# Kernel tuning notes

Measured on AMD Instinct MI355X. Metric: run time of the kernel, lower is better.

The kernel has to match this reference:

```python
import jax, jax.numpy as jnp
import numpy as np

B, CIN, HIN, WIN = 8192, 16, 6, 6
FM = 64                      # feature_maps
DK = FM // 2                 # 32
DV = FM // 2                 # 32
NH = FM // 2                 # 32 heads -> dkh = dvh = 1
OUT_CH = 5
HID = 128


def _conv2d(x, w, b, stride=1):
    # x: NCHW, w: OIHW, VALID padding (padding=(k-1)//2 = 0 for k=2)
    y = jax.lax.conv_general_dilated(
        x, w, window_strides=(stride, stride), padding='VALID',
        dimension_numbers=('NCHW', 'OIHW', 'NCHW'))
    return y + b[None, :, None, None]


def setup_inputs() -> dict:
    key = jax.random.key(0)
    ks = jax.random.split(key, 13)
    s = 0.1  # small init scale keeps softmax logits well-conditioned
    return {
        'x':      jax.random.normal(ks[0], (B, CIN, HIN, WIN), jnp.float32),
        # AugmentedConv: conv_out (out_channels - dv), qkv conv (2dk+dv), attn 1x1
        'conv_w': jax.random.normal(ks[1], (FM - DV, CIN, 2, 2), jnp.float32) * s,
        'conv_b': jax.random.normal(ks[2], (FM - DV,), jnp.float32) * s,
        'qkv_w':  jax.random.normal(ks[3], (2 * DK + DV, CIN, 2, 2), jnp.float32) * s,
        'qkv_b':  jax.random.normal(ks[4], (2 * DK + DV,), jnp.float32) * s,
        'attn_w': jax.random.normal(ks[5], (DV, DV, 1, 1), jnp.float32) * s,
        'attn_b': jax.random.normal(ks[6], (DV,), jnp.float32) * s,
        # DoubleDense: fm*5*5 -> hid -> hid//2 -> out
        'w1': jax.random.normal(ks[7], (HID, FM * 5 * 5), jnp.float32) * s,
        'b1': jax.random.normal(ks[8], (HID,), jnp.float32) * s,
        'w2': jax.random.normal(ks[9], (HID // 2, HID), jnp.float32) * s,
        'b2': jax.random.normal(ks[10], (HID // 2,), jnp.float32) * s,
        'w3': jax.random.normal(ks[11], (OUT_CH, HID // 2), jnp.float32) * s,
        'b3': jax.random.normal(ks[12], (OUT_CH,), jnp.float32) * s,
    }


def _forward(x, conv_w, conv_b, qkv_w, qkv_b, attn_w, attn_b, w1, b1, w2, b2, w3, b3):
    # ---- AugmentedConv ----
    conv_out = _conv2d(x, conv_w, conv_b)            # [B, FM-DV, 5, 5]
    qkv = _conv2d(x, qkv_w, qkv_b)                   # [B, 2DK+DV, 5, 5]
    b, _, h, w = qkv.shape
    q, k, v = jnp.split(qkv, [DK, 2 * DK], axis=1)
    dkh = DK // NH
    q = q * (dkh ** -0.5)
    flat_q = q.reshape(b, NH, dkh, h * w)            # [B, Nh, dkh, HW]
    flat_k = k.reshape(b, NH, dkh, h * w)
    flat_v = v.reshape(b, NH, DV // NH, h * w)
    # logits = q^T k over head-dim: [B, Nh, HW, HW]
    logits = jnp.einsum('bndi,bndj->bnij', flat_q, flat_k)
    weights = jax.nn.softmax(logits, axis=-1)
    # attn = weights @ v^T -> [B, Nh, HW, dvh]
    attn = jnp.einsum('bnij,bnjd->bnid', weights, flat_v.transpose(0, 1, 3, 2))
    # faithful to torch: raw reshape (B, Nh, dvh, H, W) then combine heads
    attn = attn.reshape(b, NH, DV // NH, h, w).reshape(b, DV, h, w)
    attn = _conv2d(attn, attn_w, attn_b)             # 1x1 conv
    y = jnp.concatenate([conv_out, attn], axis=1)    # [B, FM, 5, 5]
    # ---- ReLU + DoubleDense ----
    y = jax.nn.relu(y).reshape(b, -1)                # [B, FM*25]
    y = jax.nn.relu(y @ w1.T + b1)
    y = jax.nn.relu(y @ w2.T + b2)
    return y @ w3.T + b3                             # [B, OUT_CH]


def reference(x, conv_w, conv_b, qkv_w, qkv_b, attn_w, attn_b, w1, b1, w2, b2, w3, b3):
    return _forward(x, conv_w, conv_b, qkv_w, qkv_b, attn_w, attn_b,
                    w1, b1, w2, b2, w3, b3)
```

## Files before the change

kernel.cpp:

```cpp
#include <hip/hip_runtime.h>
#include <hip/hip_bf16.h>
#include <cstdint>
#include <cstddef>


typedef __attribute__((ext_vector_type(4))) float f32x4;
typedef __attribute__((ext_vector_type(8))) __bf16 bf16x8;
typedef __attribute__((ext_vector_type(4))) __bf16 bf16x4;

#define LOG2E 1.4426950408889634f

__device__ __forceinline__ float fast_exp2(float x) {
#if __has_builtin(__builtin_amdgcn_exp2f)
  return __builtin_amdgcn_exp2f(x);
#else
  return __expf(x * 0.6931471805599453f);
#endif
}

__device__ __forceinline__ f32x4 mfma16(bf16x8 a, bf16x8 b, f32x4 c) {
  return __builtin_amdgcn_mfma_f32_16x16x32_bf16(a, b, c, 0, 0, 0);
}

__global__ __launch_bounds__(256) void prep(
    const float* __restrict__ conv_w, const float* __restrict__ qkv_w,
    const float* __restrict__ w1, const float* __restrict__ w2,
    __hip_bfloat16* __restrict__ wqb, __hip_bfloat16* __restrict__ w1bp,
    __hip_bfloat16* __restrict__ w2b) {
  int i = blockIdx.x * 256 + threadIdx.x;
  if (i < 128 * 1600) {
    int n = i / 1600, r = i - n * 1600;
    int c = r & 63, p = r >> 6;
    w1bp[i] = __float2bfloat16(w1[n * 1600 + c * 25 + p]);
  }
  if (i < 8192) {
    wqb[i] = __float2bfloat16(i < 2048 ? conv_w[i] : qkv_w[i - 2048]);
    w2b[i] = __float2bfloat16(w2[i]);
  }
}

__global__ __launch_bounds__(256) void k1(
    const float* __restrict__ x,
    const float* __restrict__ conv_b, const float* __restrict__ qkv_b,
    const __hip_bfloat16* __restrict__ wqb,
    const float* __restrict__ attn_w, const float* __restrict__ attn_b,
    __hip_bfloat16* __restrict__ act) {
  const int t = threadIdx.x;
  const int lane = t & 63, wave = t >> 6;
  const int l15 = lane & 15, quad = lane >> 4;
  const int b0 = blockIdx.x * 4;

  __shared__ __align__(16) char lds_raw[6400 + 27648];
  __bf16* xs  = (__bf16*)lds_raw;
  __bf16* as_ = (__bf16*)lds_raw;
  __bf16* qs  = (__bf16*)(lds_raw + 6400);

  const float* xb = x + (size_t)b0 * 576;
#pragma unroll
  for (int i = 0; i < 9; ++i) {
    int f = t + i * 256;
    xs[f] = __float2bfloat16(xb[f]);
  }

  bf16x8 bfr[8][2];
#pragma unroll
  for (int nt = 0; nt < 8; ++nt)
#pragma unroll
    for (int ks = 0; ks < 2; ++ks)
      bfr[nt][ks] = *(const bf16x8*)((const __bf16*)wqb + (nt * 16 + l15) * 64 + ks * 32 + quad * 8);
  float bias[8];
#pragma unroll
  for (int nt = 0; nt < 8; ++nt) {
    int ch = nt * 16 + l15;
    bias[nt] = (ch < 32) ? conv_b[ch] : qkv_b[ch - 32];
  }
  __syncthreads();

  for (int mt = wave; mt < 7; mt += 4) {
    int row = mt * 16 + l15;
    int rc = row < 99 ? row : 99;
    int bl = rc / 25, pos = rc - bl * 25;
    int ii = pos / 5, jj = pos - ii * 5;
    const __bf16* xp = xs + bl * 576 + ii * 6 + jj;
    bf16x8 af[2];
#pragma unroll
    for (int ks = 0; ks < 2; ++ks) {
      const __bf16* p0 = xp + (ks * 8 + quad * 2) * 36;
      bf16x8 a;
      a[0] = p0[0];  a[1] = p0[1];  a[2] = p0[6];  a[3] = p0[7];
      a[4] = p0[36]; a[5] = p0[37]; a[6] = p0[42]; a[7] = p0[43];
      af[ks] = a;
    }
    f32x4 acc[8];
#pragma unroll
    for (int nt = 0; nt < 8; ++nt) acc[nt] = (f32x4){0.f, 0.f, 0.f, 0.f};
#pragma unroll
    for (int ks = 0; ks < 2; ++ks)
#pragma unroll
      for (int nt = 0; nt < 8; ++nt)
        acc[nt] = mfma16(af[ks], bfr[nt][ks], acc[nt]);

#pragma unroll
    for (int r = 0; r < 4; ++r) {
      int orow = mt * 16 + quad * 4 + r;
      if (orow < 100) {
        int ob = orow / 25, op = orow - ob * 25;
#pragma unroll
        for (int nt = 0; nt < 8; ++nt) {
          float v = acc[nt][r] + bias[nt];
          if (nt < 2) {
            act[((size_t)(b0 + ob) * 25 + op) * 64 + nt * 16 + l15] =
                __float2bfloat16(fmaxf(v, 0.f));
          } else {
            if (nt == 4 || nt == 5) v *= LOG2E;
            qs[(ob * 96 + (nt - 2) * 16 + l15) * 36 + op] = __float2bfloat16(v);
          }
        }
      }
    }
  }
  __syncthreads();

  {
    const int pair = t & 127, half = t >> 7;
    const int bl = pair >> 5, n = pair & 31;
    const __bf16* qp = qs + (bl * 96 + n) * 36;
    const __bf16* kp = qp + 32 * 36;
    const __bf16* vp = qp + 64 * 36;
    float kl[25], vv[25];
#pragma unroll
    for (int c4 = 0; c4 < 6; ++c4) {
      bf16x4 b = *(const bf16x4*)(kp + c4 * 4);
      bf16x4 c = *(const bf16x4*)(vp + c4 * 4);
#pragma unroll
      for (int z = 0; z < 4; ++z) {
        kl[c4 * 4 + z] = (float)b[z];
        vv[c4 * 4 + z] = (float)c[z];
      }
    }
    kl[24] = (float)kp[24]; vv[24] = (float)vp[24];

    const int i0 = half * 12;
    float qv[13];
    {
      const __bf16* qbase = qp + i0;
      bf16x4 q0 = *(const bf16x4*)(qbase);
      bf16x4 q1 = *(const bf16x4*)(qbase + 4);
      bf16x4 q2 = *(const bf16x4*)(qbase + 8);
#pragma unroll
      for (int z = 0; z < 4; ++z) {
        qv[z] = (float)q0[z]; qv[4 + z] = (float)q1[z]; qv[8 + z] = (float)q2[z];
      }
      qv[12] = (float)qbase[12];
    }

#pragma unroll
    for (int z = 0; z < 13; ++z) {
      const float qi = qv[z];
      float s0 = 0.f, s1 = 0.f, s2 = 0.f, s3 = 0.f, s4 = 0.f;
      float o0 = 0.f, o1 = 0.f, o2 = 0.f, o3 = 0.f, o4 = 0.f;
#pragma unroll
      for (int g = 0; g < 5; ++g) {
        float e0 = fast_exp2(qi * kl[g * 5 + 0]);
        float e1 = fast_exp2(qi * kl[g * 5 + 1]);
        float e2 = fast_exp2(qi * kl[g * 5 + 2]);
        float e3 = fast_exp2(qi * kl[g * 5 + 3]);
        float e4 = fast_exp2(qi * kl[g * 5 + 4]);
        s0 += e0; o0 = __builtin_fmaf(e0, vv[g * 5 + 0], o0);
        s1 += e1; o1 = __builtin_fmaf(e1, vv[g * 5 + 1], o1);
        s2 += e2; o2 = __builtin_fmaf(e2, vv[g * 5 + 2], o2);
        s3 += e3; o3 = __builtin_fmaf(e3, vv[g * 5 + 3], o3);
        s4 += e4; o4 = __builtin_fmaf(e4, vv[g * 5 + 4], o4);
      }
      float ss = ((s0 + s1) + (s2 + s3)) + s4;
      float oo = ((o0 + o1) + (o2 + o3)) + o4;
      as_[(bl * 25 + i0 + z) * 32 + n] = __float2bfloat16(oo * __builtin_amdgcn_rcpf(ss));
    }
  }
  __syncthreads();

  {
    bf16x8 bw[2]; float ab[2];
#pragma unroll
    for (int nt2 = 0; nt2 < 2; ++nt2) {
      int n = nt2 * 16 + l15;
#pragma unroll
      for (int j = 0; j < 8; ++j)
        bw[nt2][j] = (__bf16)__float2bfloat16(attn_w[n * 32 + quad * 8 + j]);
      ab[nt2] = attn_b[n];
    }
    for (int mt = wave; mt < 7; mt += 4) {
      int row = mt * 16 + l15;
      int rc = row < 99 ? row : 99;
      bf16x8 af = *(const bf16x8*)(as_ + rc * 32 + quad * 8);
      f32x4 acc[2];
#pragma unroll
      for (int nt2 = 0; nt2 < 2; ++nt2)
        acc[nt2] = mfma16(af, bw[nt2], (f32x4){0.f, 0.f, 0.f, 0.f});
#pragma unroll
      for (int r = 0; r < 4; ++r) {
        int orow = mt * 16 + quad * 4 + r;
        if (orow < 100) {
          int ob = orow / 25, op = orow - ob * 25;
#pragma unroll
          for (int nt2 = 0; nt2 < 2; ++nt2)
            act[((size_t)(b0 + ob) * 25 + op) * 64 + 32 + nt2 * 16 + l15] =
                __float2bfloat16(fmaxf(acc[nt2][r] + ab[nt2], 0.f));
        }
      }
    }
  }
}

__global__ __launch_bounds__(512) void k2(
    const __hip_bfloat16* __restrict__ act,
    const __hip_bfloat16* __restrict__ w1bp, const float* __restrict__ b1,
    const __hip_bfloat16* __restrict__ w2b, const float* __restrict__ b2,
    const float* __restrict__ w3, const float* __restrict__ b3,
    float* __restrict__ out) {
  const int t = threadIdx.x;
  const int lane = t & 63;
  const int wave = t >> 6;
  const int wm = wave >> 2;
  const int wn = wave & 3;
  const int l15 = lane & 15;
  const int quad = lane >> 4;
  const int b0 = blockIdx.x * 32;

  __shared__ __hip_bfloat16 C1s[32 * 136];
  __shared__ __hip_bfloat16 C2s[32 * 72];

  f32x4 acc0 = {0.f, 0.f, 0.f, 0.f};
  f32x4 acc1 = {0.f, 0.f, 0.f, 0.f};
  const __bf16* aptr  = (const __bf16*)act + (size_t)(b0 + wm * 16 + l15) * 1600 + quad * 8;
  const __bf16* bptr0 = (const __bf16*)w1bp + (size_t)(wn * 32 + l15) * 1600 + quad * 8;
  const __bf16* bptr1 = bptr0 + 16 * 1600;
#pragma unroll 5
  for (int k0 = 0; k0 < 1600; k0 += 32) {
    bf16x8 av  = *(const bf16x8*)(aptr + k0);
    bf16x8 bv0 = *(const bf16x8*)(bptr0 + k0);
    bf16x8 bv1 = *(const bf16x8*)(bptr1 + k0);
    acc0 = mfma16(av, bv0, acc0);
    acc1 = mfma16(av, bv1, acc1);
  }
  {
    const int col0 = wn * 32 + l15;
    const float bias0 = b1[col0];
    const float bias1 = b1[col0 + 16];
#pragma unroll
    for (int r = 0; r < 4; ++r) {
      const int row = wm * 16 + quad * 4 + r;
      C1s[row * 136 + col0]      = __float2bfloat16(fmaxf(acc0[r] + bias0, 0.f));
      C1s[row * 136 + col0 + 16] = __float2bfloat16(fmaxf(acc1[r] + bias1, 0.f));
    }
  }
  __syncthreads();

  f32x4 acc2 = {0.f, 0.f, 0.f, 0.f};
  {
    const __bf16* aL = (const __bf16*)C1s + (wm * 16 + l15) * 136 + quad * 8;
    const __bf16* bL = (const __bf16*)w2b + (wn * 16 + l15) * 128 + quad * 8;
#pragma unroll
    for (int k0 = 0; k0 < 128; k0 += 32)
      acc2 = mfma16(*(const bf16x8*)(aL + k0), *(const bf16x8*)(bL + k0), acc2);
  }
  {
    const int col = wn * 16 + l15;
    const float bias = b2[col];
#pragma unroll
    for (int r = 0; r < 4; ++r) {
      const int row = wm * 16 + quad * 4 + r;
      C2s[row * 72 + col] = __float2bfloat16(fmaxf(acc2[r] + bias, 0.f));
    }
  }
  __syncthreads();

  if (t < 160) {
    const int row = t / 5;
    const int oc = t - row * 5;
    float s = b3[oc];
#pragma unroll
    for (int k = 0; k < 64; ++k)
      s += __bfloat162float(C2s[row * 72 + k]) * w3[oc * 64 + k];
    out[(size_t)(b0 + row) * 5 + oc] = s;
  }
}

extern "C" void kernel_launch(void* const* d_in, const int* in_sizes, int n_in,
                              void* d_out, int out_size, void* d_ws, size_t ws_size,
                              hipStream_t stream) {
  const float* x      = (const float*)d_in[0];
  const float* conv_w = (const float*)d_in[1];
  const float* conv_b = (const float*)d_in[2];
  const float* qkv_w  = (const float*)d_in[3];
  const float* qkv_b  = (const float*)d_in[4];
  const float* attn_w = (const float*)d_in[5];
  const float* attn_b = (const float*)d_in[6];
  const float* w1 = (const float*)d_in[7];
  const float* b1 = (const float*)d_in[8];
  const float* w2 = (const float*)d_in[9];
  const float* b2 = (const float*)d_in[10];
  const float* w3 = (const float*)d_in[11];
  const float* b3 = (const float*)d_in[12];
  float* out = (float*)d_out;

  char* ws = (char*)d_ws;
  __hip_bfloat16* act  = (__hip_bfloat16*)ws;
  __hip_bfloat16* w1bp = (__hip_bfloat16*)(ws + 26214400);
  __hip_bfloat16* w2b  = (__hip_bfloat16*)(ws + 26624000);
  __hip_bfloat16* wqb  = (__hip_bfloat16*)(ws + 26640384);

  prep<<<dim3(800), dim3(256), 0, stream>>>(conv_w, qkv_w, w1, w2, wqb, w1bp, w2b);
  k1<<<dim3(2048), dim3(256), 0, stream>>>(x, conv_b, qkv_b, wqb, attn_w, attn_b, act);
  k2<<<dim3(256), dim3(512), 0, stream>>>(act, w1bp, b1, w2b, b2, w3, b3, out);
}
```

Before: 177.3 us.

## Fold weight prep kernel into k1 and shrink attention LDS stride

Removes the separate prep launch. The first 160 blocks of k1 now convert w1 (with its permutation) and w2 to bf16. Every block converts its conv/qkv weight fragments directly from fp32 global memory instead of reading a pre-converted buffer. The q/k/v LDS row stride drops from 36 to 28 elements, which shrinks shared memory and may raise occupancy, and the softmax loop now runs exactly 12 or 13 rows per half instead of always 13. The cost is extra fp32 loads and conversions per block, and some load imbalance on the blocks that also convert weights.

```diff
diff --git a/kernel.cpp b/kernel.cpp
--- a/kernel.cpp
+++ b/kernel.cpp
@@ -22,39 +22,37 @@
   return __builtin_amdgcn_mfma_f32_16x16x32_bf16(a, b, c, 0, 0, 0);
 }
 
-__global__ __launch_bounds__(256) void prep(
-    const float* __restrict__ conv_w, const float* __restrict__ qkv_w,
-    const float* __restrict__ w1, const float* __restrict__ w2,
-    __hip_bfloat16* __restrict__ wqb, __hip_bfloat16* __restrict__ w1bp,
-    __hip_bfloat16* __restrict__ w2b) {
-  int i = blockIdx.x * 256 + threadIdx.x;
-  if (i < 128 * 1600) {
-    int n = i / 1600, r = i - n * 1600;
-    int c = r & 63, p = r >> 6;
-    w1bp[i] = __float2bfloat16(w1[n * 1600 + c * 25 + p]);
-  }
-  if (i < 8192) {
-    wqb[i] = __float2bfloat16(i < 2048 ? conv_w[i] : qkv_w[i - 2048]);
-    w2b[i] = __float2bfloat16(w2[i]);
-  }
-}
-
 __global__ __launch_bounds__(256) void k1(
     const float* __restrict__ x,
-    const float* __restrict__ conv_b, const float* __restrict__ qkv_b,
-    const __hip_bfloat16* __restrict__ wqb,
+    const float* __restrict__ conv_w, const float* __restrict__ conv_b,
+    const float* __restrict__ qkv_w,  const float* __restrict__ qkv_b,
     const float* __restrict__ attn_w, const float* __restrict__ attn_b,
-    __hip_bfloat16* __restrict__ act) {
+    const float* __restrict__ w1, const float* __restrict__ w2,
+    __hip_bfloat16* __restrict__ act,
+    __hip_bfloat16* __restrict__ w1bp, __hip_bfloat16* __restrict__ w2b) {
   const int t = threadIdx.x;
   const int lane = t & 63, wave = t >> 6;
   const int l15 = lane & 15, quad = lane >> 4;
   const int b0 = blockIdx.x * 4;
 
-  __shared__ __align__(16) char lds_raw[6400 + 27648];
+  __shared__ __align__(16) char lds_raw[6400 + 21504];
   __bf16* xs  = (__bf16*)lds_raw;
   __bf16* as_ = (__bf16*)lds_raw;
   __bf16* qs  = (__bf16*)(lds_raw + 6400);
 
+  if (blockIdx.x < 128) {
+    const int n = blockIdx.x;
+    const float* wr = w1 + n * 1600;
+    __hip_bfloat16* wo = w1bp + n * 1600;
+    for (int o = t; o < 1600; o += 256) {
+      int c = o & 63, p = o >> 6;
+      wo[o] = __float2bfloat16(wr[c * 25 + p]);
+    }
+  } else if (blockIdx.x < 160) {
+    int i = (blockIdx.x - 128) * 256 + t;
+    w2b[i] = __float2bfloat16(w2[i]);
+  }
+
   const float* xb = x + (size_t)b0 * 576;
 #pragma unroll
   for (int i = 0; i < 9; ++i) {
@@ -63,16 +61,23 @@
   }
 
   bf16x8 bfr[8][2];
-#pragma unroll
-  for (int nt = 0; nt < 8; ++nt)
-#pragma unroll
-    for (int ks = 0; ks < 2; ++ks)
-      bfr[nt][ks] = *(const bf16x8*)((const __bf16*)wqb + (nt * 16 + l15) * 64 + ks * 32 + quad * 8);
   float bias[8];
 #pragma unroll
   for (int nt = 0; nt < 8; ++nt) {
     int ch = nt * 16 + l15;
+    const float* wrow = (ch < 32) ? (conv_w + ch * 64) : (qkv_w + (ch - 32) * 64);
     bias[nt] = (ch < 32) ? conv_b[ch] : qkv_b[ch - 32];
+#pragma unroll
+    for (int ks = 0; ks < 2; ++ks) {
+      float4 a = *(const float4*)(wrow + ks * 32 + quad * 8);
+      float4 b = *(const float4*)(wrow + ks * 32 + quad * 8 + 4);
+      bf16x8 f;
+      f[0] = (__bf16)__float2bfloat16(a.x); f[1] = (__bf16)__float2bfloat16(a.y);
+      f[2] = (__bf16)__float2bfloat16(a.z); f[3] = (__bf16)__float2bfloat16(a.w);
+      f[4] = (__bf16)__float2bfloat16(b.x); f[5] = (__bf16)__float2bfloat16(b.y);
+      f[6] = (__bf16)__float2bfloat16(b.z); f[7] = (__bf16)__float2bfloat16(b.w);
+      bfr[nt][ks] = f;
+    }
   }
   __syncthreads();
 
@@ -113,7 +118,7 @@
                 __float2bfloat16(fmaxf(v, 0.f));
           } else {
             if (nt == 4 || nt == 5) v *= LOG2E;
-            qs[(ob * 96 + (nt - 2) * 16 + l15) * 36 + op] = __float2bfloat16(v);
+            qs[(ob * 96 + (nt - 2) * 16 + l15) * 28 + op] = __float2bfloat16(v);
           }
         }
       }
@@ -124,9 +129,9 @@
   {
     const int pair = t & 127, half = t >> 7;
     const int bl = pair >> 5, n = pair & 31;
-    const __bf16* qp = qs + (bl * 96 + n) * 36;
-    const __bf16* kp = qp + 32 * 36;
-    const __bf16* vp = qp + 64 * 36;
+    const __bf16* qp = qs + (bl * 96 + n) * 28;
+    const __bf16* kp = qp + 32 * 28;
+    const __bf16* vp = qp + 64 * 28;
     float kl[25], vv[25];
 #pragma unroll
     for (int c4 = 0; c4 < 6; ++c4) {
@@ -154,8 +159,7 @@
       qv[12] = (float)qbase[12];
     }
 
-#pragma unroll
-    for (int z = 0; z < 13; ++z) {
+    auto do_i = [&](int z) {
       const float qi = qv[z];
       float s0 = 0.f, s1 = 0.f, s2 = 0.f, s3 = 0.f, s4 = 0.f;
       float o0 = 0.f, o1 = 0.f, o2 = 0.f, o3 = 0.f, o4 = 0.f;
@@ -175,6 +179,13 @@
       float ss = ((s0 + s1) + (s2 + s3)) + s4;
       float oo = ((o0 + o1) + (o2 + o3)) + o4;
       as_[(bl * 25 + i0 + z) * 32 + n] = __float2bfloat16(oo * __builtin_amdgcn_rcpf(ss));
+    };
+    if (half) {
+#pragma unroll
+      for (int z = 0; z < 13; ++z) do_i(z);
+    } else {
+#pragma unroll
+      for (int z = 0; z < 12; ++z) do_i(z);
     }
   }
   __syncthreads();
@@ -308,9 +319,8 @@
   __hip_bfloat16* act  = (__hip_bfloat16*)ws;
   __hip_bfloat16* w1bp = (__hip_bfloat16*)(ws + 26214400);
   __hip_bfloat16* w2b  = (__hip_bfloat16*)(ws + 26624000);
-  __hip_bfloat16* wqb  = (__hip_bfloat16*)(ws + 26640384);
-
-  prep<<<dim3(800), dim3(256), 0, stream>>>(conv_w, qkv_w, w1, w2, wqb, w1bp, w2b);
-  k1<<<dim3(2048), dim3(256), 0, stream>>>(x, conv_b, qkv_b, wqb, attn_w, attn_b, act);
+
+  k1<<<dim3(2048), dim3(256), 0, stream>>>(x, conv_w, conv_b, qkv_w, qkv_b,
+                                           attn_w, attn_b, w1, w2, act, w1bp, w2b);
   k2<<<dim3(256), dim3(512), 0, stream>>>(act, w1bp, b1, w2b, b2, w3, b3, out);
 }
```

Measured after the change: 214.7 us. +21.1%, slower.
